# Kernel tuning notes

Measured on AMD Instinct MI355X. Metric: run time of the kernel, lower is better.

Reference implementation:

```python
import jax, jax.numpy as jnp
import numpy as np

B, T, HID, D_IN, D_OUT = 64, 4096, 128, 22, 2


def setup_inputs() -> dict:
    key = jax.random.key(0)
    ks = jax.random.split(key, 20)
    s = 1.0 / np.sqrt(HID)
    return {
        "x": jax.random.normal(ks[0], (B, T, 11, 2), jnp.float32),
        "u": jax.random.normal(ks[1], (B, T, 2, 1), jnp.float32),
        "dt": jnp.float32(0.01),
        "theta": jax.random.normal(ks[2], (2, 2), jnp.float32),
        "H_e": jax.random.normal(ks[3], (1,), jnp.float32),
        "tau_e": 1.0 + 0.1 * jax.random.normal(ks[4], (1,), jnp.float32),
        "H_i": jax.random.normal(ks[5], (1,), jnp.float32),
        "tau_i": 1.0 + 0.1 * jax.random.normal(ks[6], (1,), jnp.float32),
        "lam1": jax.random.normal(ks[7], (1,), jnp.float32),
        "lam2": jax.random.normal(ks[8], (1,), jnp.float32),
        "lam3": jax.random.normal(ks[9], (1,), jnp.float32),
        "lam4": jax.random.normal(ks[10], (1,), jnp.float32),
        "C_f": jax.random.normal(ks[11], (2, 2), jnp.float32),
        "C_l": jax.random.normal(ks[12], (2, 2), jnp.float32),
        "C_u": jax.random.normal(ks[13], (2, 2), jnp.float32),
        "C_b": jax.random.normal(ks[14], (2, 2), jnp.float32),
        "W_ih": s * jax.random.normal(ks[15], (4 * HID, D_IN), jnp.float32),
        "W_hh": s * jax.random.normal(ks[16], (4 * HID, HID), jnp.float32),
        "b_ih": s * jax.random.normal(ks[17], (4 * HID,), jnp.float32),
        "b_hh": s * jax.random.normal(ks[18], (4 * HID,), jnp.float32),
        "W_lin": s * jax.random.normal(ks[19], (D_OUT, HID), jnp.float32),
        "b_lin": jnp.zeros((D_OUT,), jnp.float32),
    }


def _forward(x, u, dt, theta, H_e, tau_e, H_i, tau_i, lam1, lam2, lam3, lam4,
             C_f, C_l, C_u, C_b, W_ih, W_hh, b_ih, b_hh, W_lin, b_lin):
    # x: [B,T,11,2] state channels, u: [B,T,2,1] exogenous input.
    # Key insight: the per-step ODE update reads only x[:,t] (the provided
    # trajectory), never the previous ODE output, so it vectorizes over T.
    # Only the LSTM hidden/cell state is truly sequential -> lax.scan.
    sig = jax.nn.sigmoid
    Bb, Tt = x.shape[0], x.shape[1]
    I2 = jnp.eye(2, dtype=x.dtype)
    xt_theta = jnp.einsum('btn,nm->btm', x[:, :, 0, :], theta)   # [B,T,2]
    ut_theta = jnp.einsum('btn,nm->btm', u[..., 0], theta)       # [B,T,2]
    s_xt = sig(xt_theta)
    He_te = H_e / tau_e
    # torch did matmul(M, v.T).T; equivalently v @ M.T (einsum 'btn,mn->btm').
    x0 = x[:, :, 0] + dt * (x[:, :, 5] - x[:, :, 6])
    x1 = x[:, :, 1] + dt * x[:, :, 4]
    x2 = x[:, :, 2] + dt * x[:, :, 5]
    x3 = x[:, :, 3] + dt * x[:, :, 6]
    x4 = x[:, :, 4] + dt * (He_te * (jnp.einsum('btn,mn->btm', s_xt, C_f + C_l + lam1 * I2)
                                     + jnp.einsum('btn,mn->btm', ut_theta, C_u))
                            - 2.0 * x[:, :, 4] / tau_e - x[:, :, 1] / tau_e ** 2)
    x5 = x[:, :, 5] + dt * (He_te * (jnp.einsum('btn,mn->btm', s_xt, C_b + C_l)
                                     + lam2 * sig(x[:, :, 3]))
                            - 2.0 * x[:, :, 5] / tau_e - x[:, :, 2] / tau_e ** 2)
    x6 = x[:, :, 6] + dt * (H_i / tau_i * lam4 * sig(x[:, :, 7])
                            - 2.0 * x[:, :, 6] / tau_i - x[:, :, 3] / tau_i ** 2)
    x7 = x[:, :, 7] + dt * x[:, :, 8]
    x8 = x[:, :, 8] + dt * (He_te * jnp.einsum('btn,mn->btm', s_xt, C_b + C_l + lam3 * I2)
                            - 2.0 * x[:, :, 8] / tau_e - x[:, :, 7] / tau_e ** 2)
    state = jnp.stack([x0, x1, x2, x3, x4, x5, x6, x7, x8,
                       x[:, :, 9], x[:, :, 10]], axis=2)     # [B,T,11,2]
    feats = state.reshape(Bb, Tt, 22)                         # LSTM inputs

    H = W_hh.shape[1]
    # Precompute input-to-gate projection for all steps (one big GEMM).
    gates_in = jnp.einsum('bti,gi->btg', feats, W_ih) + b_ih + b_hh  # [B,T,4H]

    def step(carry, g_in):
        h, c = carry
        g = g_in + h @ W_hh.T                                 # [B,4H]
        i = sig(g[:, :H])
        f = sig(g[:, H:2 * H])
        gg = jnp.tanh(g[:, 2 * H:3 * H])
        o = sig(g[:, 3 * H:])
        c = f * c + i * gg
        h = o * jnp.tanh(c)
        return (h, c), h

    h0 = jnp.zeros((Bb, H), feats.dtype)
    _, hs = jax.lax.scan(step, (h0, h0), jnp.swapaxes(gates_in, 0, 1))
    hs = jnp.swapaxes(hs, 0, 1)                               # [B,T,H]
    out = jnp.einsum('bth,oh->bto', hs, W_lin) + b_lin        # [B,T,2]
    return out[..., None]                                     # [B,T,2,1]


def reference(x, u, dt, theta, H_e, tau_e, H_i, tau_i, lam1, lam2, lam3, lam4,
              C_f, C_l, C_u, C_b, W_ih, W_hh, b_ih, b_hh, W_lin, b_lin):
    return _forward(x, u, dt, theta, H_e, tau_e, H_i, tau_i, lam1, lam2, lam3, lam4,
                    C_f, C_l, C_u, C_b, W_ih, W_hh, b_ih, b_hh, W_lin, b_lin)
```

## Files before the change

### kernel.cpp

```cpp
#include <hip/hip_runtime.h>

#define B_   64
#define T_   4096
#define HID_ 128

typedef float f32x4 __attribute__((ext_vector_type(4)));
typedef short s16x8 __attribute__((ext_vector_type(8)));
typedef short s16x4 __attribute__((ext_vector_type(4)));

__device__ __forceinline__ float fexp2(float x){ float r; asm("v_exp_f32 %0, %1":"=v"(r):"v"(x)); return r; }
__device__ __forceinline__ float frcp (float x){ float r; asm("v_rcp_f32 %0, %1":"=v"(r):"v"(x)); return r; }
__device__ __forceinline__ unsigned short f2bf(float f){
    unsigned u = __float_as_uint(f);
    u += 0x7FFFu + ((u >> 16) & 1u);
    return (unsigned short)(u >> 16);
}
__device__ __forceinline__ float sigf(float x){
    return frcp(1.0f + fexp2(-1.44269504089f * x));
}
__device__ __forceinline__ void bar_lgkm(){
    asm volatile("s_waitcnt lgkmcnt(0)\ns_barrier" ::: "memory");
    __builtin_amdgcn_sched_barrier(0);
}

__global__ __launch_bounds__(256) void k_feats(
    const float* __restrict__ x, const float* __restrict__ u,
    const float* __restrict__ dtp, const float* __restrict__ theta,
    const float* __restrict__ He, const float* __restrict__ taue,
    const float* __restrict__ Hi, const float* __restrict__ taui,
    const float* __restrict__ l1, const float* __restrict__ l2,
    const float* __restrict__ l3, const float* __restrict__ l4,
    const float* __restrict__ Cf, const float* __restrict__ Cl,
    const float* __restrict__ Cu, const float* __restrict__ Cb,
    unsigned short* __restrict__ feats)
{
    long idx = (long)blockIdx.x * 256 + threadIdx.x;
    const float dt = dtp[0];
    const float th00 = theta[0], th01 = theta[1], th10 = theta[2], th11 = theta[3];
    const float he = He[0], te = taue[0], hi = Hi[0], ti = taui[0];
    const float L1 = l1[0], L2v = l2[0], L3 = l3[0], L4 = l4[0];
    float cf[4], cl[4], cu[4], cb[4];
    #pragma unroll
    for (int i = 0; i < 4; ++i){ cf[i]=Cf[i]; cl[i]=Cl[i]; cu[i]=Cu[i]; cb[i]=Cb[i]; }
    const float ite  = 1.f/te, iti = 1.f/ti;
    const float He_te = he*ite, ite2 = ite*ite;
    const float Hi_ti = hi*iti, iti2 = iti*iti;

    float X[22];
    const float2* xr = (const float2*)(x + idx*22);
    #pragma unroll
    for (int i = 0; i < 11; ++i){ float2 v = xr[i]; X[2*i] = v.x; X[2*i+1] = v.y; }
    float2 uv = ((const float2*)u)[idx];

    float xt0 = X[0]*th00 + X[1]*th10;
    float xt1 = X[0]*th01 + X[1]*th11;
    float ut0 = uv.x*th00 + uv.y*th10;
    float ut1 = uv.x*th01 + uv.y*th11;
    float s0 = sigf(xt0), s1 = sigf(xt1);

    float Mf00 = cf[0]+cl[0]+L1, Mf01 = cf[1]+cl[1], Mf10 = cf[2]+cl[2], Mf11 = cf[3]+cl[3]+L1;
    float Af0 = Mf00*s0 + Mf01*s1, Af1 = Mf10*s0 + Mf11*s1;
    float Au0 = cu[0]*ut0 + cu[1]*ut1, Au1 = cu[2]*ut0 + cu[3]*ut1;
    float Mb00 = cb[0]+cl[0], Mb01 = cb[1]+cl[1], Mb10 = cb[2]+cl[2], Mb11 = cb[3]+cl[3];
    float Abl0 = Mb00*s0 + Mb01*s1, Abl1 = Mb10*s0 + Mb11*s1;
    float A30 = (Mb00+L3)*s0 + Mb01*s1,  A31 = Mb10*s0 + (Mb11+L3)*s1;

    float F[22];
    F[0]  = X[0]  + dt*(X[10]-X[12]);
    F[1]  = X[1]  + dt*(X[11]-X[13]);
    F[2]  = X[2]  + dt*X[8];
    F[3]  = X[3]  + dt*X[9];
    F[4]  = X[4]  + dt*X[10];
    F[5]  = X[5]  + dt*X[11];
    F[6]  = X[6]  + dt*X[12];
    F[7]  = X[7]  + dt*X[13];
    F[8]  = X[8]  + dt*(He_te*(Af0+Au0) - 2.f*X[8]*ite  - X[2]*ite2);
    F[9]  = X[9]  + dt*(He_te*(Af1+Au1) - 2.f*X[9]*ite  - X[3]*ite2);
    F[10] = X[10] + dt*(He_te*(Abl0 + L2v*sigf(X[6])) - 2.f*X[10]*ite - X[4]*ite2);
    F[11] = X[11] + dt*(He_te*(Abl1 + L2v*sigf(X[7])) - 2.f*X[11]*ite - X[5]*ite2);
    F[12] = X[12] + dt*(Hi_ti*L4*sigf(X[14]) - 2.f*X[12]*iti - X[6]*iti2);
    F[13] = X[13] + dt*(Hi_ti*L4*sigf(X[15]) - 2.f*X[13]*iti - X[7]*iti2);
    F[14] = X[14] + dt*X[16];
    F[15] = X[15] + dt*X[17];
    F[16] = X[16] + dt*(He_te*A30 - 2.f*X[16]*ite - X[14]*ite2);
    F[17] = X[17] + dt*(He_te*A31 - 2.f*X[17]*ite - X[15]*ite2);
    F[18] = X[18]; F[19] = X[19]; F[20] = X[20]; F[21] = X[21];

    unsigned short op[32];
    #pragma unroll
    for (int s = 0; s < 4; ++s){
        #pragma unroll
        for (int e = 0; e < 8; ++e){
            int j = s*4 + (e & 3) + ((e >> 2) << 4);
            op[s*8+e] = (j < 22) ? f2bf(F[j]) : (unsigned short)0;
        }
    }
    uint4* dst = (uint4*)(feats + idx*32);
    #pragma unroll
    for (int q = 0; q < 4; ++q){
        uint4 v;
        v.x = (unsigned)op[q*8+0] | ((unsigned)op[q*8+1] << 16);
        v.y = (unsigned)op[q*8+2] | ((unsigned)op[q*8+3] << 16);
        v.z = (unsigned)op[q*8+4] | ((unsigned)op[q*8+5] << 16);
        v.w = (unsigned)op[q*8+6] | ((unsigned)op[q*8+7] << 16);
        dst[q] = v;
    }
}

__global__ __launch_bounds__(512, 1) void k_scan(
    const unsigned short* __restrict__ feats,
    const float* __restrict__ Wih, const float* __restrict__ Whh,
    const float* __restrict__ bih, const float* __restrict__ bhh,
    const float* __restrict__ Wlin, const float* __restrict__ blin,
    float* __restrict__ out)
{
    __shared__ __align__(16) unsigned short hist[16 * 576];
    __shared__ __align__(16) unsigned short fch[64 * 32];

    const int tid = threadIdx.x;
    const int w  = tid >> 6;
    const int l  = tid & 63;
    const int lm = l & 15;
    const int lg = l >> 4;
    const int gb0 = blockIdx.x * 4;
    const int ar  = lm >> 2;

    for (int i = tid; i < 16*576/2; i += 512) ((unsigned*)hist)[i] = 0u;

    const int nj = w*16 + lm;
    s16x8 bw[4][5];
    #pragma unroll
    for (int t4 = 0; t4 < 4; ++t4){
        int n = t4*128 + nj;
        #pragma unroll
        for (int kc = 0; kc < 5; ++kc){
            #pragma unroll
            for (int j = 0; j < 8; ++j){
                int k = kc*32 + lg*4 + (j & 3) + ((j >> 2) << 4);
                float wv = 0.f;
                if (kc == 0){ if (k < 22) wv = Wih[n*22 + k]; }
                else        { wv = Whh[n*128 + (k - 32)]; }
                bw[t4][kc][j] = (short)f2bf(wv);
            }
        }
    }
    s16x8 wlf[4];
    #pragma unroll
    for (int kc = 0; kc < 4; ++kc){
        #pragma unroll
        for (int j = 0; j < 8; ++j){
            int k = kc*32 + lg*4 + (j & 3) + ((j >> 2) << 4);
            wlf[kc][j] = (lm < 2) ? (short)f2bf(Wlin[lm*128 + k]) : (short)0;
        }
    }
    const float blv = blin[l & 1];

    const float L2E = 1.44269504089f;
    float nLb0, nLb1, nLb3, b2g;
    {
        float bi = bih[0*128+nj] + bhh[0*128+nj];
        float bf = bih[1*128+nj] + bhh[1*128+nj];
        float bg = bih[2*128+nj] + bhh[2*128+nj];
        float bo = bih[3*128+nj] + bhh[3*128+nj];
        nLb0 = -L2E*bi; nLb1 = -L2E*bf; nLb3 = -L2E*bo; b2g = 2.f*L2E*bg;
    }

    const int aoff = ar*144 + lg*8;
    const int khc = nj >> 5;
    const int hwoff = lg*144 + (khc*4 + ((nj >> 2) & 3))*8 + ((nj >> 4) & 1)*4 + (nj & 3);
    const int gfoff = ((lm & 3)*4 + (lm >> 2))*32 + lg*8;

    const int u_t = tid >> 4, u_b = (tid >> 2) & 3, u_q = tid & 3;
    const unsigned short* psrc = feats + ((long)(gb0 + u_b)*T_ + u_t)*32 + u_q*8;
    unsigned short* const pdst = fch + (u_t*4 + u_b)*32 + u_q*8;

    const f32x4 Z4 = {0.f, 0.f, 0.f, 0.f};

    if (tid < 256){ uint4 t0 = *(const uint4*)psrc; *(uint4*)pdst = t0; }
    uint4 pend = {0,0,0,0};
    if (tid < 256) pend = *(const uint4*)(psrc + (long)16*32);
    __syncthreads();

    f32x4 p[4][4];
    float c = 0.f;
    const int NCHK = T_/16;

    for (int chk = 0; chk < NCHK; ++chk){
        #pragma unroll
        for (int mt = 0; mt < 4; ++mt){
            s16x8 af = *(const s16x8*)(fch + mt*16*32 + gfoff);
            p[mt][0] = __builtin_amdgcn_mfma_f32_16x16x32_bf16(af, bw[0][0], Z4, 0,0,0);
            p[mt][1] = __builtin_amdgcn_mfma_f32_16x16x32_bf16(af, bw[1][0], Z4, 0,0,0);
            p[mt][2] = __builtin_amdgcn_mfma_f32_16x16x32_bf16(af, bw[2][0], Z4, 0,0,0);
            p[mt][3] = __builtin_amdgcn_mfma_f32_16x16x32_bf16(af, bw[3][0], Z4, 0,0,0);
        }
        bar_lgkm();

        if (tid < 256){
            *(uint4*)pdst = pend;
            long nk = (chk < NCHK-2) ? (chk + 2) : (NCHK-1);
            pend = *(const uint4*)(psrc + nk*16*32);
        }
        if (w >= 4 && chk > 0){
            const int mt = w - 4;
            const unsigned short* ap = hist + (mt*4 + (lm>>2))*576 + (lm&3)*144 + lg*8;
            s16x8 q0 = *(const s16x8*)(ap +  0);
            s16x8 q1 = *(const s16x8*)(ap + 32);
            s16x8 q2 = *(const s16x8*)(ap + 64);
            s16x8 q3 = *(const s16x8*)(ap + 96);
            f32x4 acc = __builtin_amdgcn_mfma_f32_16x16x32_bf16(q0, wlf[0], Z4, 0,0,0);
            acc = __builtin_amdgcn_mfma_f32_16x16x32_bf16(q1, wlf[1], acc, 0,0,0);
            acc = __builtin_amdgcn_mfma_f32_16x16x32_bf16(q2, wlf[2], acc, 0,0,0);
            acc = __builtin_amdgcn_mfma_f32_16x16x32_bf16(q3, wlf[3], acc, 0,0,0);
            if (lm < 2){
                const int tY = (chk - 1)*16 + mt*4 + lg;
                #pragma unroll
                for (int r = 0; r < 4; ++r)
                    out[((long)(gb0 + r)*T_ + tY)*2 + lm] = acc[r] + blv;
            }
        }
        bar_lgkm();

        #pragma unroll
        for (int s = 0; s < 16; ++s){
            const unsigned short* hp = hist + ((s+15)&15)*576 + aoff;
            s16x8 h1 = *(const s16x8*)(hp +  0);
            s16x8 h2 = *(const s16x8*)(hp + 32);
            s16x8 h3 = *(const s16x8*)(hp + 64);
            s16x8 h4 = *(const s16x8*)(hp + 96);

            f32x4 a0 = __builtin_amdgcn_mfma_f32_16x16x32_bf16(h1, bw[0][1], Z4, 0,0,0);
            f32x4 a1 = __builtin_amdgcn_mfma_f32_16x16x32_bf16(h1, bw[1][1], Z4, 0,0,0);
            f32x4 a2 = __builtin_amdgcn_mfma_f32_16x16x32_bf16(h1, bw[2][1], Z4, 0,0,0);
            f32x4 a3 = __builtin_amdgcn_mfma_f32_16x16x32_bf16(h1, bw[3][1], Z4, 0,0,0);
            a0 = __builtin_amdgcn_mfma_f32_16x16x32_bf16(h2, bw[0][2], a0, 0,0,0);
            a1 = __builtin_amdgcn_mfma_f32_16x16x32_bf16(h2, bw[1][2], a1, 0,0,0);
            a2 = __builtin_amdgcn_mfma_f32_16x16x32_bf16(h2, bw[2][2], a2, 0,0,0);
            a3 = __builtin_amdgcn_mfma_f32_16x16x32_bf16(h2, bw[3][2], a3, 0,0,0);
            a0 = __builtin_amdgcn_mfma_f32_16x16x32_bf16(h3, bw[0][3], a0, 0,0,0);
            a1 = __builtin_amdgcn_mfma_f32_16x16x32_bf16(h3, bw[1][3], a1, 0,0,0);
            a2 = __builtin_amdgcn_mfma_f32_16x16x32_bf16(h3, bw[2][3], a2, 0,0,0);
            a3 = __builtin_amdgcn_mfma_f32_16x16x32_bf16(h3, bw[3][3], a3, 0,0,0);
            a0 = __builtin_amdgcn_mfma_f32_16x16x32_bf16(h4, bw[0][4], a0, 0,0,0);
            a1 = __builtin_amdgcn_mfma_f32_16x16x32_bf16(h4, bw[1][4], a1, 0,0,0);
            a2 = __builtin_amdgcn_mfma_f32_16x16x32_bf16(h4, bw[2][4], a2, 0,0,0);
            a3 = __builtin_amdgcn_mfma_f32_16x16x32_bf16(h4, bw[3][4], a3, 0,0,0);

            float gi  = a0[0] + p[s>>2][0][s&3];
            float gfo = a1[0] + p[s>>2][1][s&3];
            float gg  = a2[0] + p[s>>2][2][s&3];
            float go  = a3[0] + p[s>>2][3][s&3];
            float si = frcp(1.f + fexp2(fmaf(gi,  -L2E, nLb0)));
            float sf = frcp(1.f + fexp2(fmaf(gfo, -L2E, nLb1)));
            float so = frcp(1.f + fexp2(fmaf(go,  -L2E, nLb3)));
            float eg = fexp2(fmaf(gg, 2.f*L2E, b2g));
            float tg_ = fmaf(-2.f, frcp(1.f + eg), 1.f);
            c = sf*c + si*tg_;
            float ec = fexp2(c * (2.f*L2E));
            float tc_ = fmaf(-2.f, frcp(1.f + ec), 1.f);
            float h = so * tc_;

            unsigned hp2;
            asm("v_cvt_pk_bf16_f32 %0, %1, %1" : "=v"(hp2) : "v"(h));
            hist[s*576 + hwoff] = (unsigned short)hp2;

            bar_lgkm();
        }
    }

    if (w >= 4){
        const int mt = w - 4;
        const unsigned short* ap = hist + (mt*4 + (lm>>2))*576 + (lm&3)*144 + lg*8;
        s16x8 q0 = *(const s16x8*)(ap +  0);
        s16x8 q1 = *(const s16x8*)(ap + 32);
        s16x8 q2 = *(const s16x8*)(ap + 64);
        s16x8 q3 = *(const s16x8*)(ap + 96);
        f32x4 acc = __builtin_amdgcn_mfma_f32_16x16x32_bf16(q0, wlf[0], Z4, 0,0,0);
        acc = __builtin_amdgcn_mfma_f32_16x16x32_bf16(q1, wlf[1], acc, 0,0,0);
        acc = __builtin_amdgcn_mfma_f32_16x16x32_bf16(q2, wlf[2], acc, 0,0,0);
        acc = __builtin_amdgcn_mfma_f32_16x16x32_bf16(q3, wlf[3], acc, 0,0,0);
        if (lm < 2){
            const int tY = (T_ - 16) + mt*4 + lg;
            #pragma unroll
            for (int r = 0; r < 4; ++r)
                out[((long)(gb0 + r)*T_ + tY)*2 + lm] = acc[r] + blv;
        }
    }
}

extern "C" void kernel_launch(void* const* d_in, const int* in_sizes, int n_in,
                              void* d_out, int out_size, void* d_ws, size_t ws_size,
                              hipStream_t stream)
{
    const float* x     = (const float*)d_in[0];
    const float* u     = (const float*)d_in[1];
    const float* dtp   = (const float*)d_in[2];
    const float* theta = (const float*)d_in[3];
    const float* He    = (const float*)d_in[4];
    const float* taue  = (const float*)d_in[5];
    const float* Hi    = (const float*)d_in[6];
    const float* taui  = (const float*)d_in[7];
    const float* l1    = (const float*)d_in[8];
    const float* l2    = (const float*)d_in[9];
    const float* l3    = (const float*)d_in[10];
    const float* l4    = (const float*)d_in[11];
    const float* Cf    = (const float*)d_in[12];
    const float* Cl    = (const float*)d_in[13];
    const float* Cu    = (const float*)d_in[14];
    const float* Cb    = (const float*)d_in[15];
    const float* Wih   = (const float*)d_in[16];
    const float* Whh   = (const float*)d_in[17];
    const float* bih   = (const float*)d_in[18];
    const float* bhh   = (const float*)d_in[19];
    const float* Wlin  = (const float*)d_in[20];
    const float* blin  = (const float*)d_in[21];

    unsigned short* feats = (unsigned short*)d_ws;

    k_feats<<<(B_*T_)/256, 256, 0, stream>>>(x,u,dtp,theta,He,taue,Hi,taui,
                                             l1,l2,l3,l4,Cf,Cl,Cu,Cb,feats);
    k_scan<<<16, 512, 0, stream>>>(feats, Wih, Whh, bih, bhh, Wlin, blin, (float*)d_out);
}
```

Before: 1.768 ms.

## Overlap next chunk's input-projection MFMAs with recurrent LSTM steps

The input-to-gate projection for the next 16-step chunk is now computed one MFMA per recurrent step, interleaved into the step loop, instead of as a block of 16 MFMAs at each chunk boundary. Ping-pong register buffers (pA/pB) hold the current and next chunk's projections, and the chunk boundary no longer needs a separate barrier for the projection phase. This takes projection work off the serial critical path, filling MFMA idle slots during the latency-bound recurrence, at the cost of doubling the projection accumulator registers.

```diff
diff --git a/kernel.cpp b/kernel.cpp
--- a/kernel.cpp
+++ b/kernel.cpp
@@ -175,32 +175,27 @@
     unsigned short* const pdst = fch + (u_t*4 + u_b)*32 + u_q*8;
 
     const f32x4 Z4 = {0.f, 0.f, 0.f, 0.f};
+    const int NCHK = T_/16;
 
     if (tid < 256){ uint4 t0 = *(const uint4*)psrc; *(uint4*)pdst = t0; }
+    __syncthreads();
+    f32x4 pA[4][4], pB[4][4];
+    #pragma unroll
+    for (int mt = 0; mt < 4; ++mt){
+        s16x8 af = *(const s16x8*)(fch + mt*512 + gfoff);
+        pA[mt][0] = __builtin_amdgcn_mfma_f32_16x16x32_bf16(af, bw[0][0], Z4, 0,0,0);
+        pA[mt][1] = __builtin_amdgcn_mfma_f32_16x16x32_bf16(af, bw[1][0], Z4, 0,0,0);
+        pA[mt][2] = __builtin_amdgcn_mfma_f32_16x16x32_bf16(af, bw[2][0], Z4, 0,0,0);
+        pA[mt][3] = __builtin_amdgcn_mfma_f32_16x16x32_bf16(af, bw[3][0], Z4, 0,0,0);
+    }
     uint4 pend = {0,0,0,0};
     if (tid < 256) pend = *(const uint4*)(psrc + (long)16*32);
     __syncthreads();
 
-    f32x4 p[4][4];
     float c = 0.f;
-    const int NCHK = T_/16;
-
-    for (int chk = 0; chk < NCHK; ++chk){
-        #pragma unroll
-        for (int mt = 0; mt < 4; ++mt){
-            s16x8 af = *(const s16x8*)(fch + mt*16*32 + gfoff);
-            p[mt][0] = __builtin_amdgcn_mfma_f32_16x16x32_bf16(af, bw[0][0], Z4, 0,0,0);
-            p[mt][1] = __builtin_amdgcn_mfma_f32_16x16x32_bf16(af, bw[1][0], Z4, 0,0,0);
-            p[mt][2] = __builtin_amdgcn_mfma_f32_16x16x32_bf16(af, bw[2][0], Z4, 0,0,0);
-            p[mt][3] = __builtin_amdgcn_mfma_f32_16x16x32_bf16(af, bw[3][0], Z4, 0,0,0);
-        }
-        bar_lgkm();
-
-        if (tid < 256){
-            *(uint4*)pdst = pend;
-            long nk = (chk < NCHK-2) ? (chk + 2) : (NCHK-1);
-            pend = *(const uint4*)(psrc + nk*16*32);
-        }
+
+    auto boundary = [&](int chk){
+        if (tid < 256) *(uint4*)pdst = pend;
         if (w >= 4 && chk > 0){
             const int mt = w - 4;
             const unsigned short* ap = hist + (mt*4 + (lm>>2))*576 + (lm&3)*144 + lg*8;
@@ -219,8 +214,15 @@
                     out[((long)(gb0 + r)*T_ + tY)*2 + lm] = acc[r] + blv;
             }
         }
+        {
+            long nk = (chk < NCHK-2) ? (chk + 2) : (NCHK-1);
+            if (tid < 256) pend = *(const uint4*)(psrc + nk*(long)(16*32));
+        }
         bar_lgkm();
-
+    };
+
+    auto steps = [&](f32x4 (&P)[4][4], f32x4 (&PN)[4][4]){
+        s16x8 afg;
         #pragma unroll
         for (int s = 0; s < 16; ++s){
             const unsigned short* hp = hist + ((s+15)&15)*576 + aoff;
@@ -228,6 +230,9 @@
             s16x8 h2 = *(const s16x8*)(hp + 32);
             s16x8 h3 = *(const s16x8*)(hp + 64);
             s16x8 h4 = *(const s16x8*)(hp + 96);
+            if ((s & 3) == 0) afg = *(const s16x8*)(fch + (s>>2)*512 + gfoff);
+            PN[s>>2][s&3] = __builtin_amdgcn_mfma_f32_16x16x32_bf16(afg, bw[s&3][0], Z4, 0,0,0);
+            __builtin_amdgcn_sched_barrier(0);
 
             f32x4 a0 = __builtin_amdgcn_mfma_f32_16x16x32_bf16(h1, bw[0][1], Z4, 0,0,0);
             f32x4 a1 = __builtin_amdgcn_mfma_f32_16x16x32_bf16(h1, bw[1][1], Z4, 0,0,0);
@@ -246,10 +251,10 @@
             a2 = __builtin_amdgcn_mfma_f32_16x16x32_bf16(h4, bw[2][4], a2, 0,0,0);
             a3 = __builtin_amdgcn_mfma_f32_16x16x32_bf16(h4, bw[3][4], a3, 0,0,0);
 
-            float gi  = a0[0] + p[s>>2][0][s&3];
-            float gfo = a1[0] + p[s>>2][1][s&3];
-            float gg  = a2[0] + p[s>>2][2][s&3];
-            float go  = a3[0] + p[s>>2][3][s&3];
+            float gi  = a0[0] + P[s>>2][0][s&3];
+            float gfo = a1[0] + P[s>>2][1][s&3];
+            float gg  = a2[0] + P[s>>2][2][s&3];
+            float go  = a3[0] + P[s>>2][3][s&3];
             float si = frcp(1.f + fexp2(fmaf(gi,  -L2E, nLb0)));
             float sf = frcp(1.f + fexp2(fmaf(gfo, -L2E, nLb1)));
             float so = frcp(1.f + fexp2(fmaf(go,  -L2E, nLb3)));
@@ -266,6 +271,11 @@
 
             bar_lgkm();
         }
+    };
+
+    for (int c2 = 0; c2 < NCHK/2; ++c2){
+        boundary(2*c2);       steps(pA, pB);
+        boundary(2*c2 + 1);   steps(pB, pA);
     }
 
     if (w >= 4){
```

Measured after the change: 1.666 ms. 5.8% less time.
